# Kernel tuning notes

Measured on AMD Instinct MI355X. Metric: run time of the kernel, lower is better.

Reference implementation:

```python
import jax, jax.numpy as jnp
import numpy as np

NHEAD = 4
LAYER_TYPES = ["self", "cross", "self", "cross", "semantic_subspace_cross"]


def _ln(x):
    m = jnp.mean(x, axis=-1, keepdims=True)
    v = jnp.var(x, axis=-1, keepdims=True)
    return (x - m) / jnp.sqrt(v + 1e-5)


def _attn(x, source, q_mask, kv_mask, qW, kW, vW, mW, w1, w2):
    # Faithful GeometryAttentionLayer forward (pe=None, sinusoidal branch).
    bs, L, C = x.shape
    dim = C // NHEAD
    qw = (x @ qW).reshape(bs, L, NHEAD, dim)
    kw = (source @ kW).reshape(bs, -1, NHEAD, dim)
    vw = (source @ vW).reshape(bs, -1, NHEAD, dim)
    a = jnp.einsum('nlhd,nshd->nlsh', qw, kw)
    if q_mask is not None:
        bad = q_mask[:, :, None, None] & (~kv_mask)[:, None, :, None]
        a = jnp.where(bad, -jnp.inf, a)
    a = jax.nn.softmax(a / jnp.sqrt(jnp.asarray(dim, x.dtype)), axis=2)
    o = jnp.einsum('nlsh,nshd->nlhd', a, vw).reshape(bs, L, C)
    msg = _ln(o @ mW)
    h = jnp.concatenate([x, msg], axis=-1)
    msg = _ln(jnp.maximum(h @ w1, 0.0) @ w2)
    return x + msg


def setup_inputs() -> dict:
    key = jax.random.key(0)
    ks = jax.random.split(key, 24)
    B, N, C, D2 = 2, 2048, 256, 384
    G, Lp, nL = 16, 512, len(LAYER_TYPES)
    inp = {
        'src_feat': jax.random.normal(ks[0], (B, N, C), jnp.float32),
        'tgt_feat': jax.random.normal(ks[1], (B, N, C), jnp.float32),
        's_pcd': jax.random.normal(ks[2], (B, N, 3), jnp.float32),
        't_pcd': jax.random.normal(ks[3], (B, N, 3), jnp.float32),
        'src_mask': jnp.ones((B, N), bool),
        'tgt_mask': jnp.ones((B, N), bool),
        'src_sub_ind_padded': jax.random.randint(ks[4], (G, Lp), 0, N + 1),
        'tgt_sub_ind_padded': jax.random.randint(ks[5], (G, Lp), 0, N + 1),
        'src_sub_ind_padded_mask': jnp.ones((G, Lp), bool),
        'tgt_sub_ind_padded_mask': jnp.ones((G, Lp), bool),
        'semantic_masks_valid': jnp.ones((G,), bool),
        'src_2dfeat': jax.random.normal(ks[6], (B, N, D2), jnp.float32),
        'tgt_2dfeat': jax.random.normal(ks[7], (B, N, D2), jnp.float32),
        'data': 0,
        'dinoW': jax.random.normal(ks[8], (D2, C), jnp.float32) / np.sqrt(D2),
        'qW': jax.random.normal(ks[9], (nL, C, C), jnp.float32) / np.sqrt(C),
        'kW': jax.random.normal(ks[10], (nL, C, C), jnp.float32) / np.sqrt(C),
        'vW': jax.random.normal(ks[11], (nL, C, C), jnp.float32) / np.sqrt(C),
        'mW': jax.random.normal(ks[12], (nL, C, C), jnp.float32) / np.sqrt(C),
        'w1': jax.random.normal(ks[13], (nL, 2 * C, 2 * C), jnp.float32) / np.sqrt(2 * C),
        'w2': jax.random.normal(ks[14], (nL, 2 * C, C), jnp.float32) / np.sqrt(2 * C),
    }
    return inp


def reference(src_feat, tgt_feat, s_pcd, t_pcd, src_mask, tgt_mask,
              src_sub_ind_padded, tgt_sub_ind_padded,
              src_sub_ind_padded_mask, tgt_sub_ind_padded_mask,
              semantic_masks_valid, src_2dfeat, tgt_2dfeat, data,
              dinoW, qW, kW, vW, mW, w1, w2):
    src2 = src_2dfeat @ dinoW
    tgt2 = tgt_2dfeat @ dinoW
    s_sem = t_sem = None
    for i, name in enumerate(LAYER_TYPES):
        P = (qW[i], kW[i], vW[i], mW[i], w1[i], w2[i])
        if name == 'self':
            src_feat = src_feat + src2
            tgt_feat = tgt_feat + tgt2
            src_feat = _attn(src_feat, src_feat, src_mask, src_mask, *P)
            tgt_feat = _attn(tgt_feat, tgt_feat, tgt_mask, tgt_mask, *P)
        elif name == 'cross':
            src_feat = _attn(src_feat, tgt_feat, src_mask, tgt_mask, *P)
            tgt_feat = _attn(tgt_feat, src_feat, tgt_mask, src_mask, *P)
        else:  # semantic_subspace_cross
            B, N, C = src_feat.shape
            G = src_sub_ind_padded.shape[0]
            mask_num = G // B
            se = jnp.repeat(src_feat[:, None], mask_num, axis=1).reshape(G, N, C)
            te = jnp.repeat(tgt_feat[:, None], mask_num, axis=1).reshape(G, N, C)
            # boolean-select valid semantic groups (all valid in this config,
            # so fixed-size nonzero is exact)
            vidx = jnp.nonzero(semantic_masks_valid, size=G, fill_value=0)[0]
            se, te = se[vidx], te[vidx]
            si, ti = src_sub_ind_padded[vidx], tgt_sub_ind_padded[vidx]
            sm, tm = src_sub_ind_padded_mask[vidx], tgt_sub_ind_padded_mask[vidx]
            # append zero row so pad index N gathers zeros
            se = jnp.concatenate([se, jnp.zeros_like(se[:, :1])], axis=1)
            te = jnp.concatenate([te, jnp.zeros_like(te[:, :1])], axis=1)
            ssub = jnp.take_along_axis(se, si[:, :, None], axis=1)
            tsub = jnp.take_along_axis(te, ti[:, :, None], axis=1)
            s_sem = _attn(ssub, tsub, ~sm, ~tm, *P)
            t_sem = _attn(tsub, ssub, ~tm, ~sm, *P)
    return (src_feat, tgt_feat, s_sem, t_sem)
```

## Files before the change

kernel.cpp:

```cpp
#include <hip/hip_runtime.h>
#include <hip/hip_bf16.h>
#include <cstdint>
#include <cstddef>


typedef __attribute__((ext_vector_type(8))) short bf16x8;
typedef __attribute__((ext_vector_type(4))) float f32x4;

__device__ __forceinline__ float b2f(unsigned short u) {
  union { unsigned int i; float f; } v; v.i = ((unsigned int)u) << 16; return v.f;
}
__device__ __forceinline__ unsigned short f2b(float f) {
  __hip_bfloat16 h = __float2bfloat16(f);
  union { __hip_bfloat16 h; unsigned short u; } v; v.h = h; return v.u;
}
__device__ __forceinline__ unsigned int pk2(float a, float b) {
  return (unsigned int)f2b(a) | ((unsigned int)f2b(b) << 16);
}
__device__ __forceinline__ float fexp2(float x) {
#if __has_builtin(__builtin_amdgcn_exp2f)
  return __builtin_amdgcn_exp2f(x);
#else
  float r; asm("v_exp_f32 %0, %1" : "=v"(r) : "v"(x)); return r;
#endif
}

__global__ __launch_bounds__(256) void k_probe(int* __restrict__ flag,
                                               const unsigned short* __restrict__ w,
                                               int n) {
  __shared__ int ok[256];
  const int t = threadIdx.x;
  int good = 1;
  for (int i = t; i < n; i += 256) {
    float v = fabsf(b2f(w[i]));
    if (!(v < 1e3f)) good = 0;
  }
  ok[t] = good;
  __syncthreads();
  for (int s = 128; s; s >>= 1) {
    if (t < s) ok[t] &= ok[t + s];
    __syncthreads();
  }
  if (t == 0) *flag = ok[0];
}

__global__ __launch_bounds__(256) void k_load2(float* __restrict__ dF,
                                               unsigned short* __restrict__ dB,
                                               const void* __restrict__ src,
                                               int n4, const int* __restrict__ flag) {
  int i = blockIdx.x * 256 + threadIdx.x;
  if (i >= n4) return;
  float4 f;
  if (*flag) {
    ushort4 u = ((const ushort4*)src)[i];
    f.x = b2f(u.x); f.y = b2f(u.y); f.z = b2f(u.z); f.w = b2f(u.w);
  } else {
    f = ((const float4*)src)[i];
  }
  ((float4*)dF)[i] = f;
  ushort4 o; o.x = f2b(f.x); o.y = f2b(f.y); o.z = f2b(f.z); o.w = f2b(f.w);
  ((ushort4*)dB)[i] = o;
}

__global__ __launch_bounds__(256) void k_loadb(unsigned short* __restrict__ dB,
                                               const void* __restrict__ src,
                                               int n4, const int* __restrict__ flag) {
  int i = blockIdx.x * 256 + threadIdx.x;
  if (i >= n4) return;
  if (*flag) {
    ((ushort4*)dB)[i] = ((const ushort4*)src)[i];
    return;
  }
  float4 f = ((const float4*)src)[i];
  ushort4 o; o.x = f2b(f.x); o.y = f2b(f.y); o.z = f2b(f.z); o.w = f2b(f.w);
  ((ushort4*)dB)[i] = o;
}

__global__ __launch_bounds__(256) void k_store(void* __restrict__ out, size_t off,
                                               const float* __restrict__ src,
                                               int n4, const int* __restrict__ flag) {
  int i = blockIdx.x * 256 + threadIdx.x;
  if (i >= n4) return;
  float4 f = ((const float4*)src)[i];
  if (*flag) {
    ushort4 u; u.x = f2b(f.x); u.y = f2b(f.y); u.z = f2b(f.z); u.w = f2b(f.w);
    ((ushort4*)((unsigned short*)out + off))[i] = u;
  } else {
    ((float4*)((float*)out + off))[i] = f;
  }
}

__global__ __launch_bounds__(256) void k_add_dino(float* __restrict__ xF,
                                                  unsigned short* __restrict__ xB,
                                                  const unsigned short* __restrict__ addB,
                                                  int n4) {
  int i = blockIdx.x * 256 + threadIdx.x;
  if (i >= n4) return;
  float4 a = ((const float4*)xF)[i];
  ushort4 u = ((const ushort4*)addB)[i];
  a.x += b2f(u.x); a.y += b2f(u.y); a.z += b2f(u.z); a.w += b2f(u.w);
  ((float4*)xF)[i] = a;
  ushort4 o; o.x = f2b(a.x); o.y = f2b(a.y); o.z = f2b(a.z); o.w = f2b(a.w);
  ((ushort4*)xB)[i] = o;
}

__global__ __launch_bounds__(256) void k_wt(unsigned short* __restrict__ Wt,
                                            const void* __restrict__ W,
                                            int K, int N, int zStride,
                                            const int* __restrict__ flag) {
  __shared__ float tile[32][33];
  const int isbf = *flag;
  const int z = blockIdx.z;
  const unsigned short* Wb = (const unsigned short*)W + (size_t)z * K * N;
  const float* Wf = (const float*)W + (size_t)z * K * N;
  unsigned short* Wo = Wt + (size_t)z * zStride;
  const int KS = K >> 5;
  const int nx = blockIdx.x * 32, ky = blockIdx.y * 32;
  const int tx = threadIdx.x & 31, ty = threadIdx.x >> 5;
#pragma unroll
  for (int i = 0; i < 4; ++i) {
    int k = ky + ty + i * 8;
    float v = isbf ? b2f(Wb[(size_t)k * N + nx + tx]) : Wf[(size_t)k * N + nx + tx];
    tile[ty + i * 8][tx] = v;
  }
  __syncthreads();
  const int kstep = ky >> 5;
  const int lanehi = (tx >> 3) << 4;
  const int e = tx & 7;
#pragma unroll
  for (int i = 0; i < 4; ++i) {
    int nn = ty + i * 8;
    int n_ = nx + nn;
    size_t idx = ((((size_t)(n_ >> 4) * KS + kstep) << 6) + (lanehi + (n_ & 15))) * 8 + e;
    Wo[idx] = f2b(tile[tx][nn]);
  }
}

template<int KTOT>
__global__ __launch_bounds__(256, 4) void k_gmm(unsigned short* __restrict__ Y, int ldy,
                                                const unsigned short* __restrict__ A1, int lda1,
                                                const unsigned short* __restrict__ A2, int lda2,
                                                int K1,
                                                const unsigned short* __restrict__ Wt,
                                                int relu, int rowOff, int rowXor,
                                                int xorColStart, int qkvLog2L) {
  constexpr int KS = KTOT >> 5;
  const int tid = threadIdx.x;
  const int wq = tid >> 6, lane = tid & 63;
  const int l16 = lane & 15, quad = lane >> 4;
  const int gx = gridDim.x;
  const int nwg = gx * gridDim.y;
  const int lid = blockIdx.y * gx + blockIdx.x;
  const int w = (lid & 7) * (nwg >> 3) + (lid >> 3);
  const int n0 = (w % gx) * 64, m0 = (w / gx) * 64;
  const int row = m0 + wq * 16 + l16;
  int arow = rowOff + row;
  if (n0 >= xorColStart) arow ^= rowXor;

  const unsigned short* Wb0 = Wt + ((size_t)(n0 >> 4) * KS << 6) * 8 + (size_t)lane * 8;

  f32x4 acc[4];
#pragma unroll
  for (int i = 0; i < 4; ++i) acc[i] = (f32x4){0.f, 0.f, 0.f, 0.f};

  auto ldA = [&](int k0) -> bf16x8 {
    const unsigned short* ap = (k0 < K1)
        ? (A1 + (size_t)arow * lda1 + k0)
        : (A2 + (size_t)arow * lda2 + (k0 - K1));
    return *(const bf16x8*)(ap + quad * 8);
  };
  auto ldB = [&](int k0, int nb) -> bf16x8 {
    return *(const bf16x8*)(Wb0 + ((size_t)nb * KS + (k0 >> 5)) * 512);
  };

  bf16x8 a0 = ldA(0), a1;
  bf16x8 b0[4], b1[4];
#pragma unroll
  for (int nb = 0; nb < 4; ++nb) b0[nb] = ldB(0, nb);

#pragma unroll
  for (int k0 = 0; k0 < KTOT; k0 += 64) {
    a1 = ldA(k0 + 32);
#pragma unroll
    for (int nb = 0; nb < 4; ++nb) b1[nb] = ldB(k0 + 32, nb);
#pragma unroll
    for (int nb = 0; nb < 4; ++nb)
      acc[nb] = __builtin_amdgcn_mfma_f32_16x16x32_bf16(a0, b0[nb], acc[nb], 0, 0, 0);
    if (k0 + 64 < KTOT) {
      a0 = ldA(k0 + 64);
#pragma unroll
      for (int nb = 0; nb < 4; ++nb) b0[nb] = ldB(k0 + 64, nb);
    }
#pragma unroll
    for (int nb = 0; nb < 4; ++nb)
      acc[nb] = __builtin_amdgcn_mfma_f32_16x16x32_bf16(a1, b1[nb], acc[nb], 0, 0, 0);
  }

  if (qkvLog2L) {
    const int Lm = (1 << qkvLog2L) - 1;
    const int sel = n0 >> 8;
    const int hh = (n0 >> 6) & 3;
    unsigned short* base = Y + (size_t)sel * ((size_t)gridDim.y << 14);
#pragma unroll
    for (int r = 0; r < 4; ++r) {
      const int rr = m0 + wq * 16 + quad * 4 + r;
      const int tok = rr & Lm;
      const int hi = ((rr >> qkvLog2L) << 2) + hh;
      unsigned short* yp = base + ((((size_t)hi << qkvLog2L) + tok) << 6) + l16;
#pragma unroll
      for (int nb = 0; nb < 4; ++nb) yp[nb * 16] = f2b(acc[nb][r]);
    }
  } else {
#pragma unroll
    for (int r = 0; r < 4; ++r) {
      unsigned short* yp = Y + (size_t)(m0 + wq * 16 + quad * 4 + r) * ldy + n0;
#pragma unroll
      for (int nb = 0; nb < 4; ++nb) {
        float v = acc[nb][r];
        if (relu) v = fmaxf(v, 0.f);
        yp[nb * 16 + l16] = f2b(v);
      }
    }
  }
}

__device__ __forceinline__ void row_stats(float4 v, float& mean, float& inv) {
  float s  = v.x + v.y + v.z + v.w;
  float s2 = fmaf(v.x, v.x, fmaf(v.y, v.y, fmaf(v.z, v.z, v.w * v.w)));
#pragma unroll
  for (int off = 32; off >= 1; off >>= 1) {
    s  += __shfl_xor(s,  off, 64);
    s2 += __shfl_xor(s2, off, 64);
  }
  mean = s * (1.f / 256.f);
  float var = s2 * (1.f / 256.f) - mean * mean;
  inv = rsqrtf(var + 1e-5f);
}

template<int KTOT>
__global__ __launch_bounds__(256, 4) void k_gmm_ln(unsigned short* __restrict__ Yb,
                                                   float* __restrict__ xF,
                                                   void* __restrict__ outp, size_t outOff,
                                                   const unsigned short* __restrict__ xBres,
                                                   const unsigned short* __restrict__ A1,
                                                   int lda1,
                                                   const unsigned short* __restrict__ Wt,
                                                   int mode, const int* __restrict__ flag) {
  constexpr int KS = KTOT >> 5;
  __shared__ float Ot[16][260];
  const int tid = threadIdx.x;
  const int wq = tid >> 6, lane = tid & 63;
  const int l16 = lane & 15, quad = lane >> 4;
  const int nwg = gridDim.x;
  const int lid = blockIdx.x;
  const int w = (lid & 7) * (nwg >> 3) + (lid >> 3);
  const int R0 = w * 16;

  const unsigned short* Wb0 = Wt + ((size_t)(wq * 4) * KS << 6) * 8 + (size_t)lane * 8;
  const unsigned short* Ap = A1 + (size_t)(R0 + l16) * lda1;

  f32x4 acc[4];
#pragma unroll
  for (int i = 0; i < 4; ++i) acc[i] = (f32x4){0.f, 0.f, 0.f, 0.f};

  auto ldA = [&](int k0) -> bf16x8 { return *(const bf16x8*)(Ap + k0 + quad * 8); };
  auto ldB = [&](int k0, int nb) -> bf16x8 {
    return *(const bf16x8*)(Wb0 + ((size_t)nb * KS + (k0 >> 5)) * 512);
  };

  bf16x8 a0 = ldA(0), a1;
  bf16x8 b0[4], b1[4];
#pragma unroll
  for (int nb = 0; nb < 4; ++nb) b0[nb] = ldB(0, nb);

#pragma unroll
  for (int k0 = 0; k0 < KTOT; k0 += 64) {
    a1 = ldA(k0 + 32);
#pragma unroll
    for (int nb = 0; nb < 4; ++nb) b1[nb] = ldB(k0 + 32, nb);
#pragma unroll
    for (int nb = 0; nb < 4; ++nb)
      acc[nb] = __builtin_amdgcn_mfma_f32_16x16x32_bf16(a0, b0[nb], acc[nb], 0, 0, 0);
    if (k0 + 64 < KTOT) {
      a0 = ldA(k0 + 64);
#pragma unroll
      for (int nb = 0; nb < 4; ++nb) b0[nb] = ldB(k0 + 64, nb);
    }
#pragma unroll
    for (int nb = 0; nb < 4; ++nb)
      acc[nb] = __builtin_amdgcn_mfma_f32_16x16x32_bf16(a1, b1[nb], acc[nb], 0, 0, 0);
  }

#pragma unroll
  for (int nb = 0; nb < 4; ++nb)
#pragma unroll
    for (int r = 0; r < 4; ++r)
      Ot[quad * 4 + r][wq * 64 + nb * 16 + l16] = acc[nb][r];
  __syncthreads();

#pragma unroll
  for (int rr = 0; rr < 4; ++rr) {
    const int row = rr * 4 + wq;
    float4 v = *(const float4*)&Ot[row][lane * 4];
    float mean, inv; row_stats(v, mean, inv);
    float4 nv;
    nv.x = (v.x - mean) * inv; nv.y = (v.y - mean) * inv;
    nv.z = (v.z - mean) * inv; nv.w = (v.w - mean) * inv;
    const size_t gr = (size_t)(R0 + row) * 256 + lane * 4;
    if (mode == 1) {
      float4 xv = *(const float4*)(xF + gr);
      float4 rs;
      rs.x = xv.x + nv.x; rs.y = xv.y + nv.y; rs.z = xv.z + nv.z; rs.w = xv.w + nv.w;
      *(float4*)(xF + gr) = rs;
      ushort4 u; u.x = f2b(rs.x); u.y = f2b(rs.y); u.z = f2b(rs.z); u.w = f2b(rs.w);
      *(ushort4*)(Yb + gr) = u;
    } else {
      ushort4 xu = *(const ushort4*)(xBres + gr);
      float4 rs;
      rs.x = b2f(xu.x) + nv.x; rs.y = b2f(xu.y) + nv.y;
      rs.z = b2f(xu.z) + nv.z; rs.w = b2f(xu.w) + nv.w;
      if (*flag) {
        ushort4 u; u.x = f2b(rs.x); u.y = f2b(rs.y); u.z = f2b(rs.z); u.w = f2b(rs.w);
        *(ushort4*)((unsigned short*)outp + outOff + gr) = u;
      } else {
        *(float4*)((float*)outp + outOff + gr) = rs;
      }
    }
  }
}

__global__ __launch_bounds__(256, 4) void k_mprojc(unsigned short* __restrict__ msgB,
                                                   const float* __restrict__ pO,
                                                   const float* __restrict__ pML,
                                                   int lgL, int split, int NHt,
                                                   const unsigned short* __restrict__ Wt) {
  constexpr int KS = 8;
  __shared__ __align__(16) char smem[16640];
  unsigned short* At = (unsigned short*)smem;
  float (*Ot)[260] = (float (*)[260])smem;
  const int tid = threadIdx.x;
  const int wq = tid >> 6, lane = tid & 63;
  const int l16 = lane & 15, quad = lane >> 4;
  const int nwg = gridDim.x;
  const int lid = blockIdx.x;
  const int w = (lid & 7) * (nwg >> 3) + (lid >> 3);
  const int R0 = w * 16;
  const int L = 1 << lgL, Lm = L - 1;

  {
    const int i = tid >> 4;
    const int c = tid & 15;
    const int gr = R0 + i;
    const int n = gr >> lgL;
    const int tok = gr & Lm;
    const int nh = n * 4 + (c >> 2);
    float M = -1e30f;
    for (int sp = 0; sp < split; ++sp)
      M = fmaxf(M, pML[(((size_t)sp * NHt + nh) * L + tok) * 2]);
    float4 a0 = {0,0,0,0}, a1 = {0,0,0,0}, a2 = {0,0,0,0}, a3 = {0,0,0,0};
    float lsum = 0.f;
    for (int sp = 0; sp < split; ++sp) {
      const float* pml = pML + (((size_t)sp * NHt + nh) * L + tok) * 2;
      float e = fexp2(pml[0] - M);
      lsum = fmaf(pml[1], e, lsum);
      const float4* po = (const float4*)(pO + (((size_t)sp * NHt + nh) * L + tok) * 64
                                         + (c & 3) * 16);
      float4 v0 = po[0], v1 = po[1], v2 = po[2], v3 = po[3];
      a0.x = fmaf(v0.x, e, a0.x); a0.y = fmaf(v0.y, e, a0.y);
      a0.z = fmaf(v0.z, e, a0.z); a0.w = fmaf(v0.w, e, a0.w);
      a1.x = fmaf(v1.x, e, a1.x); a1.y = fmaf(v1.y, e, a1.y);
      a1.z = fmaf(v1.z, e, a1.z); a1.w = fmaf(v1.w, e, a1.w);
      a2.x = fmaf(v2.x, e, a2.x); a2.y = fmaf(v2.y, e, a2.y);
      a2.z = fmaf(v2.z, e, a2.z); a2.w = fmaf(v2.w, e, a2.w);
      a3.x = fmaf(v3.x, e, a3.x); a3.y = fmaf(v3.y, e, a3.y);
      a3.z = fmaf(v3.z, e, a3.z); a3.w = fmaf(v3.w, e, a3.w);
    }
    float inv = 1.0f / lsum;
    union { unsigned short us[8]; uint4 v; } p0, p1;
    p0.us[0] = f2b(a0.x * inv); p0.us[1] = f2b(a0.y * inv);
    p0.us[2] = f2b(a0.z * inv); p0.us[3] = f2b(a0.w * inv);
    p0.us[4] = f2b(a1.x * inv); p0.us[5] = f2b(a1.y * inv);
    p0.us[6] = f2b(a1.z * inv); p0.us[7] = f2b(a1.w * inv);
    p1.us[0] = f2b(a2.x * inv); p1.us[1] = f2b(a2.y * inv);
    p1.us[2] = f2b(a2.z * inv); p1.us[3] = f2b(a2.w * inv);
    p1.us[4] = f2b(a3.x * inv); p1.us[5] = f2b(a3.y * inv);
    p1.us[6] = f2b(a3.z * inv); p1.us[7] = f2b(a3.w * inv);
    const int u0 = (2 * c) ^ (i & 7);
    const int u1 = (2 * c + 1) ^ (i & 7);
    *(uint4*)&At[((i << 5) + u0) * 8] = p0.v;
    *(uint4*)&At[((i << 5) + u1) * 8] = p1.v;
  }
  __syncthreads();

  const unsigned short* Wb0 = Wt + ((size_t)(wq * 4) * KS << 6) * 8 + (size_t)lane * 8;
  f32x4 acc[4];
#pragma unroll
  for (int i = 0; i < 4; ++i) acc[i] = (f32x4){0.f, 0.f, 0.f, 0.f};

  auto ldA = [&](int k0) -> bf16x8 {
    const int u = (k0 >> 3) + quad;
    return *(const bf16x8*)&At[((l16 << 5) + (u ^ (l16 & 7))) * 8];
  };
  auto ldB = [&](int k0, int nb) -> bf16x8 {
    return *(const bf16x8*)(Wb0 + ((size_t)nb * KS + (k0 >> 5)) * 512);
  };

  bf16x8 b0[4], b1[4];
#pragma unroll
  for (int nb = 0; nb < 4; ++nb) b0[nb] = ldB(0, nb);
#pragma unroll
  for (int k0 = 0; k0 < 256; k0 += 64) {
#pragma unroll
    for (int nb = 0; nb < 4; ++nb) b1[nb] = ldB(k0 + 32, nb);
    bf16x8 a0 = ldA(k0);
#pragma unroll
    for (int nb = 0; nb < 4; ++nb)
      acc[nb] = __builtin_amdgcn_mfma_f32_16x16x32_bf16(a0, b0[nb], acc[nb], 0, 0, 0);
    if (k0 + 64 < 256) {
#pragma unroll
      for (int nb = 0; nb < 4; ++nb) b0[nb] = ldB(k0 + 64, nb);
    }
    bf16x8 a1 = ldA(k0 + 32);
#pragma unroll
    for (int nb = 0; nb < 4; ++nb)
      acc[nb] = __builtin_amdgcn_mfma_f32_16x16x32_bf16(a1, b1[nb], acc[nb], 0, 0, 0);
  }
  __syncthreads();

#pragma unroll
  for (int nb = 0; nb < 4; ++nb)
#pragma unroll
    for (int r = 0; r < 4; ++r)
      Ot[quad * 4 + r][wq * 64 + nb * 16 + l16] = acc[nb][r];
  __syncthreads();

#pragma unroll
  for (int rr = 0; rr < 4; ++rr) {
    const int row = rr * 4 + wq;
    float4 v = *(const float4*)&Ot[row][lane * 4];
    float mean, inv; row_stats(v, mean, inv);
    ushort4 u;
    u.x = f2b((v.x - mean) * inv); u.y = f2b((v.y - mean) * inv);
    u.z = f2b((v.z - mean) * inv); u.w = f2b((v.w - mean) * inv);
    *(ushort4*)(msgB + (size_t)(R0 + row) * 256 + lane * 4) = u;
  }
}

__global__ __launch_bounds__(512, 4) void k_attn_p(float* __restrict__ pO,
                                                   float* __restrict__ pML,
                                                   const unsigned short* __restrict__ QKV,
                                                   unsigned long long kOff,
                                                   int L, int S, int chunk) {
  __shared__ __align__(16) char smem[34816];
  unsigned short* Kl = (unsigned short*)smem;
  unsigned short (*Vt)[64][72] = (unsigned short (*)[64][72])(smem + 16384);
  const int tid = threadIdx.x;
  const int wq = tid >> 6, lane = tid & 63;
  const int l16 = lane & 15, quad = lane >> 4;
  const int q0 = blockIdx.x * 256;
  const int nh = blockIdx.y, NHt = gridDim.y;
  const int s0 = blockIdx.z * chunk;
  const float S2 = 0.18033688f;

  const unsigned short* Qh = QKV + (size_t)nh * L * 64;
  const unsigned short* Kh = QKV + kOff + (size_t)nh * S * 64;
  const unsigned short* Vh = QKV + 2 * kOff + (size_t)nh * S * 64;

  bf16x8 qa[2][2];
#pragma unroll
  for (int qb = 0; qb < 2; ++qb) {
    const unsigned short* qp = Qh + (size_t)(q0 + (qb * 8 + wq) * 16 + l16) * 64;
    qa[qb][0] = *(const bf16x8*)(qp + quad * 8);
    qa[qb][1] = *(const bf16x8*)(qp + 32 + quad * 8);
  }

  const short ONE = (short)0x3F80;
  const bf16x8 onesv = (bf16x8){ONE, ONE, ONE, ONE, ONE, ONE, ONE, ONE};

  f32x4 acc[2][4];
  f32x4 lacc[2];
#pragma unroll
  for (int qb = 0; qb < 2; ++qb) {
#pragma unroll
    for (int i = 0; i < 4; ++i) acc[qb][i] = (f32x4){0.f, 0.f, 0.f, 0.f};
    lacc[qb] = (f32x4){0.f, 0.f, 0.f, 0.f};
  }
  float m_[2] = {-1e30f, -1e30f};

  const int skey = tid >> 3;
  const int sdh0 = (tid & 7) * 8;
  const int kidx = (((skey >> 4) * 2 + (sdh0 >> 5)) * 64 +
                    (((sdh0 >> 3) & 3) * 16) + ((skey & 15) ^ (tid & 7))) * 8;
  const int krd0 = lane ^ quad;
  const int krd1 = lane ^ (4 | quad);
  const int vdh0 = wq * 8;
  const int pc = ((lane >> 5) << 5) + (((lane >> 2) & 3) << 3)
               + (((lane >> 4) & 1) << 2) + (lane & 3);

  uint4 kv = *(const uint4*)(Kh + (size_t)(s0 + skey) * 64 + sdh0);
  uint4 va = *(const uint4*)(Vh + (size_t)(s0 + lane) * 64 + vdh0);
  *(uint4*)&Kl[kidx] = kv;
  {
    const unsigned short* pv = (const unsigned short*)&va;
#pragma unroll
    for (int i = 0; i < 8; ++i) Vt[0][vdh0 + i][pc] = pv[i];
  }
  if (chunk > 64) {
    kv = *(const uint4*)(Kh + (size_t)(s0 + 64 + skey) * 64 + sdh0);
    va = *(const uint4*)(Vh + (size_t)(s0 + 64 + lane) * 64 + vdh0);
  }
  __syncthreads();

  int cur = 0;
  for (int t = 0; t < chunk; t += 64) {
    f32x4 sc[2][4];
    const unsigned short* Klc = Kl + cur * 4096;
    __builtin_amdgcn_s_setprio(1);
#pragma unroll
    for (int kb = 0; kb < 4; ++kb) {
      bf16x8 kf0 = *(const bf16x8*)&Klc[((kb * 2 + 0) * 64 + krd0) * 8];
      bf16x8 kf1 = *(const bf16x8*)&Klc[((kb * 2 + 1) * 64 + krd1) * 8];
#pragma unroll
      for (int qb = 0; qb < 2; ++qb) {
        f32x4 z = (f32x4){0.f, 0.f, 0.f, 0.f};
        z = __builtin_amdgcn_mfma_f32_16x16x32_bf16(kf0, qa[qb][0], z, 0, 0, 0);
        z = __builtin_amdgcn_mfma_f32_16x16x32_bf16(kf1, qa[qb][1], z, 0, 0, 0);
        sc[qb][kb] = z;
      }
    }
    __builtin_amdgcn_s_setprio(0);
    if (t + 64 < chunk) {
      *(uint4*)&Kl[(cur ^ 1) * 4096 + kidx] = kv;
      const unsigned short* pv = (const unsigned short*)&va;
#pragma unroll
      for (int i = 0; i < 8; ++i) Vt[cur ^ 1][vdh0 + i][pc] = pv[i];
    }
    if (t + 128 < chunk) {
      kv = *(const uint4*)(Kh + (size_t)(s0 + t + 128 + skey) * 64 + sdh0);
      va = *(const uint4*)(Vh + (size_t)(s0 + t + 128 + lane) * 64 + vdh0);
    }
    union { bf16x8 v; unsigned int w[4]; } ps0[2], ps1[2];
#pragma unroll
    for (int qb = 0; qb < 2; ++qb) {
      f32x4 mv01, mv;
#pragma unroll
      for (int r = 0; r < 4; ++r) mv01[r] = fmaxf(sc[qb][0][r], sc[qb][1][r]);
#pragma unroll
      for (int r = 0; r < 4; ++r) mv[r] = fmaxf(mv01[r], fmaxf(sc[qb][2][r], sc[qb][3][r]));
      float mx = fmaxf(fmaxf(mv[0], mv[1]), fmaxf(mv[2], mv[3])) * S2;
      mx = fmaxf(mx, __shfl_xor(mx, 16));
      mx = fmaxf(mx, __shfl_xor(mx, 32));
      float mn;
      if (__all(mx <= m_[qb] + 8.f)) {
        mn = m_[qb];
      } else {
        mn = fmaxf(m_[qb], mx);
        float alpha = fexp2(m_[qb] - mn);
        m_[qb] = mn;
#pragma unroll
        for (int r = 0; r < 4; ++r) lacc[qb][r] *= alpha;
#pragma unroll
        for (int nb = 0; nb < 4; ++nb)
#pragma unroll
          for (int r = 0; r < 4; ++r) acc[qb][nb][r] *= alpha;
      }
#pragma unroll
      for (int kb = 0; kb < 4; ++kb)
#pragma unroll
        for (int r = 0; r < 4; ++r)
          sc[qb][kb][r] = fexp2(fmaf(sc[qb][kb][r], S2, -mn));
      ps0[qb].w[0] = pk2(sc[qb][0][0], sc[qb][0][1]);
      ps0[qb].w[1] = pk2(sc[qb][0][2], sc[qb][0][3]);
      ps0[qb].w[2] = pk2(sc[qb][1][0], sc[qb][1][1]);
      ps0[qb].w[3] = pk2(sc[qb][1][2], sc[qb][1][3]);
      ps1[qb].w[0] = pk2(sc[qb][2][0], sc[qb][2][1]);
      ps1[qb].w[1] = pk2(sc[qb][2][2], sc[qb][2][3]);
      ps1[qb].w[2] = pk2(sc[qb][3][0], sc[qb][3][1]);
      ps1[qb].w[3] = pk2(sc[qb][3][2], sc[qb][3][3]);
    }
    __builtin_amdgcn_s_setprio(1);
#pragma unroll
    for (int db = 0; db < 4; ++db) {
      bf16x8 vb0 = *(const bf16x8*)&Vt[cur][db * 16 + l16][quad * 8];
      bf16x8 vb1 = *(const bf16x8*)&Vt[cur][db * 16 + l16][32 + quad * 8];
#pragma unroll
      for (int qb = 0; qb < 2; ++qb) {
        acc[qb][db] = __builtin_amdgcn_mfma_f32_16x16x32_bf16(vb0, ps0[qb].v, acc[qb][db], 0, 0, 0);
        acc[qb][db] = __builtin_amdgcn_mfma_f32_16x16x32_bf16(vb1, ps1[qb].v, acc[qb][db], 0, 0, 0);
      }
    }
#pragma unroll
    for (int qb = 0; qb < 2; ++qb) {
      lacc[qb] = __builtin_amdgcn_mfma_f32_16x16x32_bf16(onesv, ps0[qb].v, lacc[qb], 0, 0, 0);
      lacc[qb] = __builtin_amdgcn_mfma_f32_16x16x32_bf16(onesv, ps1[qb].v, lacc[qb], 0, 0, 0);
    }
    __builtin_amdgcn_s_setprio(0);
    __syncthreads();
    cur ^= 1;
  }

  float* Ot = (float*)smem;
#pragma unroll
  for (int qb = 0; qb < 2; ++qb) {
#pragma unroll
    for (int pass = 0; pass < 2; ++pass) {
      __syncthreads();
      if ((wq >> 2) == pass) {
#pragma unroll
        for (int db = 0; db < 4; ++db)
          *(f32x4*)&Ot[(size_t)((wq & 3) * 16 + l16) * 68 + db * 16 + quad * 4] = acc[qb][db];
      }
      __syncthreads();
      if ((wq >> 2) == pass) {
#pragma unroll
        for (int i = 0; i < 16; ++i) {
          const int row = q0 + (qb * 8 + wq) * 16 + i;
          pO[((size_t)(blockIdx.z * NHt + nh) * L + row) * 64 + lane] =
              Ot[(size_t)((wq & 3) * 16 + i) * 68 + lane];
        }
      }
    }
  }
  if (quad == 0) {
#pragma unroll
    for (int qb = 0; qb < 2; ++qb) {
      float* pml = pML + ((size_t)(blockIdx.z * NHt + nh) * L +
                          q0 + (qb * 8 + wq) * 16 + l16) * 2;
      pml[0] = m_[qb]; pml[1] = lacc[qb][0];
    }
  }
}

__global__ __launch_bounds__(256) void k_gather2(unsigned short* __restrict__ dst,
                                                 const float* __restrict__ sF,
                                                 const int* __restrict__ sIdx,
                                                 const int* __restrict__ tIdx) {
  const int row = blockIdx.x * 4 + (threadIdx.x >> 6);
  const int t = threadIdx.x & 63;
  const int half = row >> 13;
  const int r = row & 8191;
  const int g = r >> 9;
  const int b = g >> 3;
  const int id = half ? tIdx[r] : sIdx[r];
  float4 v = {0.f, 0.f, 0.f, 0.f};
  if ((unsigned)id < 2048u) {
    const float* base = sF + (size_t)(half * 2 + b) * 524288;
    v = ((const float4*)(base + (size_t)id * 256))[t];
  }
  ushort4 u; u.x = f2b(v.x); u.y = f2b(v.y); u.z = f2b(v.z); u.w = f2b(v.w);
  ((ushort4*)(dst + (size_t)row * 256))[t] = u;
}

extern "C" void kernel_launch(void* const* d_in, const int* in_sizes, int n_in,
                              void* d_out, int out_size, void* d_ws, size_t ws_size,
                              hipStream_t stream) {
  const void* src_feat = d_in[0];
  const void* tgt_feat = d_in[1];
  const int* s_sub = (const int*)d_in[6];
  const int* t_sub = (const int*)d_in[7];
  const void* src2d = d_in[11];
  const void* tgt2d = d_in[12];
  const void* dinoW = d_in[14];
  const void* qW = d_in[15];
  const void* kW = d_in[16];
  const void* vW = d_in[17];
  const void* mW = d_in[18];
  const void* w1 = d_in[19];
  const void* w2 = d_in[20];

  const int BIG = 1 << 30;
  char* p = (char*)d_ws;
  int* dflag = (int*)p;                       p += 256;
  float* sF = (float*)p;                      p += 4194304;
  float* tF = (float*)p;                      p += 4194304;
  unsigned short* sB    = (unsigned short*)p; p += 2097152;
  unsigned short* tB    = (unsigned short*)p; p += 2097152;
  unsigned short* s2B   = (unsigned short*)p; p += 2097152;
  unsigned short* t2B   = (unsigned short*)p; p += 2097152;
  unsigned short* d2B   = (unsigned short*)p; p += 3145728;
  unsigned short* sSubB = (unsigned short*)p; p += 4194304;
  unsigned short* tSubB = (unsigned short*)p; p += 4194304;
  unsigned short* qkvB  = (unsigned short*)p;
  unsigned short* msgB  = (unsigned short*)(p + 8388608);
  p += 25165824;
  unsigned short* hB    = (unsigned short*)p;
  p += 25165824;
  unsigned short* WtD   = (unsigned short*)p; p += 196608;
  unsigned short* WtQKV = (unsigned short*)p; p += 1966080;
  unsigned short* WtM   = (unsigned short*)p; p += 655360;
  unsigned short* WtW1  = (unsigned short*)p; p += 2621440;
  unsigned short* WtW2  = (unsigned short*)p; p += 1310720;
  float* pO  = (float*)p;                     p += 33554432;
  float* pML = (float*)p;                     p += 2097152;

  k_probe<<<1, 256, 0, stream>>>(dflag, (const unsigned short*)qW, 4096);

  k_wt<<<dim3(8, 12, 1), 256, 0, stream>>>(WtD, dinoW, 384, 256, 0, dflag);
  k_wt<<<dim3(8, 8, 5), 256, 0, stream>>>(WtQKV,          qW, 256, 256, 196608, dflag);
  k_wt<<<dim3(8, 8, 5), 256, 0, stream>>>(WtQKV + 65536,  kW, 256, 256, 196608, dflag);
  k_wt<<<dim3(8, 8, 5), 256, 0, stream>>>(WtQKV + 131072, vW, 256, 256, 196608, dflag);
  k_wt<<<dim3(8, 8, 5), 256, 0, stream>>>(WtM, mW, 256, 256, 65536, dflag);
  k_wt<<<dim3(16, 16, 5), 256, 0, stream>>>(WtW1, w1, 512, 512, 262144, dflag);
  k_wt<<<dim3(8, 16, 5), 256, 0, stream>>>(WtW2, w2, 512, 256, 131072, dflag);

  auto attnB = [&](int l, const unsigned short* Abase, int rowOff, int rowXor,
                   int M, int L, int S, int split, int NHt,
                   float* xF, unsigned short* xB, size_t outOff) {
    const int lg = (L == 2048) ? 11 : 9;
    k_gmm<256><<<dim3(12, M / 64), 256, 0, stream>>>(
        qkvB, 768, Abase, 256, Abase, 256, 256,
        WtQKV + (size_t)l * 196608, 0, rowOff, rowXor, 256, lg);
    const int chunk = S / split;
    k_attn_p<<<dim3(L / 256, NHt, split), 512, 0, stream>>>(
        pO, pML, qkvB, (unsigned long long)M * 256, L, S, chunk);
    k_mprojc<<<M / 16, 256, 0, stream>>>(msgB, pO, pML, lg, split, NHt,
                                         WtM + (size_t)l * 65536);
    k_gmm<512><<<dim3(8, M / 64), 256, 0, stream>>>(
        hB, 512, xB, 256, msgB, 256, 256, WtW1 + (size_t)l * 262144, 1, 0, 0, BIG, 0);
    if (xF) k_gmm_ln<512><<<M / 16, 256, 0, stream>>>(
        xB, xF, nullptr, 0, nullptr, hB, 512, WtW2 + (size_t)l * 131072, 1, dflag);
    else    k_gmm_ln<512><<<M / 16, 256, 0, stream>>>(
        nullptr, nullptr, d_out, outOff, xB, hB, 512, WtW2 + (size_t)l * 131072, 2, dflag);
  };

  k_load2<<<1024, 256, 0, stream>>>(sF, sB, src_feat, 262144, dflag);
  k_load2<<<1024, 256, 0, stream>>>(tF, tB, tgt_feat, 262144, dflag);
  k_loadb<<<1536, 256, 0, stream>>>(d2B, src2d, 393216, dflag);
  k_gmm<384><<<dim3(4, 64), 256, 0, stream>>>(s2B, 256, d2B, 384, d2B, 384, 384,
                                              WtD, 0, 0, 0, BIG, 0);
  k_loadb<<<1536, 256, 0, stream>>>(d2B, tgt2d, 393216, dflag);
  k_gmm<384><<<dim3(4, 64), 256, 0, stream>>>(t2B, 256, d2B, 384, d2B, 384, 384,
                                              WtD, 0, 0, 0, BIG, 0);

  k_add_dino<<<2048, 256, 0, stream>>>(sF, sB, s2B, 524288);
  attnB(0, sB, 0, 0, 8192, 2048, 2048, 4, 16, sF, sB, 0);
  attnB(1, sB, 0,    4096, 4096, 2048, 2048, 8, 8, sF, sB, 0);
  attnB(1, sB, 4096, 4096, 4096, 2048, 2048, 8, 8, tF, tB, 0);
  k_add_dino<<<2048, 256, 0, stream>>>(sF, sB, s2B, 524288);
  attnB(2, sB, 0, 0, 8192, 2048, 2048, 4, 16, sF, sB, 0);
  attnB(3, sB, 0,    4096, 4096, 2048, 2048, 8, 8, sF, sB, 0);
  attnB(3, sB, 4096, 4096, 4096, 2048, 2048, 8, 8, tF, tB, 0);
  k_gather2<<<4096, 256, 0, stream>>>(sSubB, sF, s_sub, t_sub);
  attnB(4, sSubB, 0, 8192, 16384, 512, 512, 2, 128, nullptr, sSubB, 2097152);

  k_store<<<2048, 256, 0, stream>>>(d_out, 0, sF, 524288, dflag);
}
```

Baseline: 738.1 us.

## Give each wave a full 16x256 row tile so layernorm runs in registers

The two GEMM+layernorm kernels now have each wave compute 16 rows across all 256 output columns, so a block covers 64 rows instead of 16. Row statistics are reduced in registers with 16-lane shuffles, which removes the LDS staging buffer and its barrier before the layernorm. The aim is to reuse each A fragment across 16 N-blocks and drop the shared-memory round trip. In exchange there are 64 accumulator registers per lane, the old double-buffered prefetch is gone, the grid is four times smaller, and the output stores become scalar 2- and 4-byte writes instead of vector stores.

```diff
diff --git a/kernel.cpp b/kernel.cpp
--- a/kernel.cpp
+++ b/kernel.cpp
@@ -224,11 +224,19 @@
   }
 }
 
-__device__ __forceinline__ void row_stats(float4 v, float& mean, float& inv) {
-  float s  = v.x + v.y + v.z + v.w;
-  float s2 = fmaf(v.x, v.x, fmaf(v.y, v.y, fmaf(v.z, v.z, v.w * v.w)));
-#pragma unroll
-  for (int off = 32; off >= 1; off >>= 1) {
+__device__ __forceinline__ void ln_reg(const f32x4 acc[4][4], int r,
+                                       float& mean, float& inv) {
+  float s = 0.f, s2 = 0.f;
+#pragma unroll
+  for (int cb = 0; cb < 4; ++cb)
+#pragma unroll
+    for (int nb = 0; nb < 4; ++nb) {
+      float v = acc[cb][nb][r];
+      s += v;
+      s2 = fmaf(v, v, s2);
+    }
+#pragma unroll
+  for (int off = 8; off >= 1; off >>= 1) {
     s  += __shfl_xor(s,  off, 64);
     s2 += __shfl_xor(s2, off, 64);
   }
@@ -247,85 +255,58 @@
                                                    const unsigned short* __restrict__ Wt,
                                                    int mode, const int* __restrict__ flag) {
   constexpr int KS = KTOT >> 5;
-  __shared__ float Ot[16][260];
   const int tid = threadIdx.x;
   const int wq = tid >> 6, lane = tid & 63;
   const int l16 = lane & 15, quad = lane >> 4;
   const int nwg = gridDim.x;
   const int lid = blockIdx.x;
   const int w = (lid & 7) * (nwg >> 3) + (lid >> 3);
-  const int R0 = w * 16;
-
-  const unsigned short* Wb0 = Wt + ((size_t)(wq * 4) * KS << 6) * 8 + (size_t)lane * 8;
-  const unsigned short* Ap = A1 + (size_t)(R0 + l16) * lda1;
-
-  f32x4 acc[4];
-#pragma unroll
-  for (int i = 0; i < 4; ++i) acc[i] = (f32x4){0.f, 0.f, 0.f, 0.f};
-
-  auto ldA = [&](int k0) -> bf16x8 { return *(const bf16x8*)(Ap + k0 + quad * 8); };
-  auto ldB = [&](int k0, int nb) -> bf16x8 {
-    return *(const bf16x8*)(Wb0 + ((size_t)nb * KS + (k0 >> 5)) * 512);
-  };
-
-  bf16x8 a0 = ldA(0), a1;
-  bf16x8 b0[4], b1[4];
-#pragma unroll
-  for (int nb = 0; nb < 4; ++nb) b0[nb] = ldB(0, nb);
-
-#pragma unroll
-  for (int k0 = 0; k0 < KTOT; k0 += 64) {
-    a1 = ldA(k0 + 32);
-#pragma unroll
-    for (int nb = 0; nb < 4; ++nb) b1[nb] = ldB(k0 + 32, nb);
-#pragma unroll
-    for (int nb = 0; nb < 4; ++nb)
-      acc[nb] = __builtin_amdgcn_mfma_f32_16x16x32_bf16(a0, b0[nb], acc[nb], 0, 0, 0);
-    if (k0 + 64 < KTOT) {
-      a0 = ldA(k0 + 64);
-#pragma unroll
-      for (int nb = 0; nb < 4; ++nb) b0[nb] = ldB(k0 + 64, nb);
-    }
-#pragma unroll
-    for (int nb = 0; nb < 4; ++nb)
-      acc[nb] = __builtin_amdgcn_mfma_f32_16x16x32_bf16(a1, b1[nb], acc[nb], 0, 0, 0);
-  }
-
-#pragma unroll
-  for (int nb = 0; nb < 4; ++nb)
-#pragma unroll
-    for (int r = 0; r < 4; ++r)
-      Ot[quad * 4 + r][wq * 64 + nb * 16 + l16] = acc[nb][r];
-  __syncthreads();
-
-#pragma unroll
-  for (int rr = 0; rr < 4; ++rr) {
-    const int row = rr * 4 + wq;
-    float4 v = *(const float4*)&Ot[row][lane * 4];
-    float mean, inv; row_stats(v, mean, inv);
-    float4 nv;
-    nv.x = (v.x - mean) * inv; nv.y = (v.y - mean) * inv;
-    nv.z = (v.z - mean) * inv; nv.w = (v.w - mean) * inv;
-    const size_t gr = (size_t)(R0 + row) * 256 + lane * 4;
-    if (mode == 1) {
-      float4 xv = *(const float4*)(xF + gr);
-      float4 rs;
-      rs.x = xv.x + nv.x; rs.y = xv.y + nv.y; rs.z = xv.z + nv.z; rs.w = xv.w + nv.w;
-      *(float4*)(xF + gr) = rs;
-      ushort4 u; u.x = f2b(rs.x); u.y = f2b(rs.y); u.z = f2b(rs.z); u.w = f2b(rs.w);
-      *(ushort4*)(Yb + gr) = u;
-    } else {
-      ushort4 xu = *(const ushort4*)(xBres + gr);
-      float4 rs;
-      rs.x = b2f(xu.x) + nv.x; rs.y = b2f(xu.y) + nv.y;
-      rs.z = b2f(xu.z) + nv.z; rs.w = b2f(xu.w) + nv.w;
-      if (*flag) {
-        ushort4 u; u.x = f2b(rs.x); u.y = f2b(rs.y); u.z = f2b(rs.z); u.w = f2b(rs.w);
-        *(ushort4*)((unsigned short*)outp + outOff + gr) = u;
-      } else {
-        *(float4*)((float*)outp + outOff + gr) = rs;
-      }
-    }
+  const int R0 = w * 64;
+
+  const unsigned short* Ap = A1 + (size_t)(R0 + wq * 16 + l16) * lda1;
+  const unsigned short* Wb0 = Wt + (size_t)lane * 8;
+
+  f32x4 acc[4][4];
+#pragma unroll
+  for (int cb = 0; cb < 4; ++cb)
+#pragma unroll
+    for (int nb = 0; nb < 4; ++nb) acc[cb][nb] = (f32x4){0.f, 0.f, 0.f, 0.f};
+
+#pragma unroll
+  for (int cb = 0; cb < 4; ++cb) {
+#pragma unroll
+    for (int k0 = 0; k0 < KTOT; k0 += 32) {
+      bf16x8 a = *(const bf16x8*)(Ap + k0 + quad * 8);
+#pragma unroll
+      for (int nb = 0; nb < 4; ++nb) {
+        bf16x8 b = *(const bf16x8*)(Wb0 +
+            (((size_t)(cb * 4 + nb) * KS + (k0 >> 5)) << 9));
+        acc[cb][nb] = __builtin_amdgcn_mfma_f32_16x16x32_bf16(a, b, acc[cb][nb], 0, 0, 0);
+      }
+    }
+  }
+
+#pragma unroll
+  for (int r = 0; r < 4; ++r) {
+    float mean, inv;
+    ln_reg(acc, r, mean, inv);
+    const int row = R0 + wq * 16 + quad * 4 + r;
+#pragma unroll
+    for (int cb = 0; cb < 4; ++cb)
+#pragma unroll
+      for (int nb = 0; nb < 4; ++nb) {
+        const float nv = (acc[cb][nb][r] - mean) * inv;
+        const size_t gr = (size_t)row * 256 + cb * 64 + nb * 16 + l16;
+        if (mode == 1) {
+          float rs = xF[gr] + nv;
+          xF[gr] = rs;
+          Yb[gr] = f2b(rs);
+        } else {
+          float rs = b2f(xBres[gr]) + nv;
+          if (*flag) ((unsigned short*)outp)[outOff + gr] = f2b(rs);
+          else       ((float*)outp)[outOff + gr] = rs;
+        }
+      }
   }
 }
 
@@ -335,20 +316,19 @@
                                                    int lgL, int split, int NHt,
                                                    const unsigned short* __restrict__ Wt) {
   constexpr int KS = 8;
-  __shared__ __align__(16) char smem[16640];
-  unsigned short* At = (unsigned short*)smem;
-  float (*Ot)[260] = (float (*)[260])smem;
+  __shared__ __align__(16) unsigned short At[64 * 32 * 8];
   const int tid = threadIdx.x;
   const int wq = tid >> 6, lane = tid & 63;
   const int l16 = lane & 15, quad = lane >> 4;
   const int nwg = gridDim.x;
   const int lid = blockIdx.x;
   const int w = (lid & 7) * (nwg >> 3) + (lid >> 3);
-  const int R0 = w * 16;
+  const int R0 = w * 64;
   const int L = 1 << lgL, Lm = L - 1;
 
-  {
-    const int i = tid >> 4;
+#pragma unroll
+  for (int it = 0; it < 4; ++it) {
+    const int i = it * 16 + (tid >> 4);
     const int c = tid & 15;
     const int gr = R0 + i;
     const int n = gr >> lgL;
@@ -392,57 +372,40 @@
   }
   __syncthreads();
 
-  const unsigned short* Wb0 = Wt + ((size_t)(wq * 4) * KS << 6) * 8 + (size_t)lane * 8;
-  f32x4 acc[4];
-#pragma unroll
-  for (int i = 0; i < 4; ++i) acc[i] = (f32x4){0.f, 0.f, 0.f, 0.f};
-
-  auto ldA = [&](int k0) -> bf16x8 {
-    const int u = (k0 >> 3) + quad;
-    return *(const bf16x8*)&At[((l16 << 5) + (u ^ (l16 & 7))) * 8];
-  };
-  auto ldB = [&](int k0, int nb) -> bf16x8 {
-    return *(const bf16x8*)(Wb0 + ((size_t)nb * KS + (k0 >> 5)) * 512);
-  };
-
-  bf16x8 b0[4], b1[4];
-#pragma unroll
-  for (int nb = 0; nb < 4; ++nb) b0[nb] = ldB(0, nb);
-#pragma unroll
-  for (int k0 = 0; k0 < 256; k0 += 64) {
-#pragma unroll
-    for (int nb = 0; nb < 4; ++nb) b1[nb] = ldB(k0 + 32, nb);
-    bf16x8 a0 = ldA(k0);
-#pragma unroll
-    for (int nb = 0; nb < 4; ++nb)
-      acc[nb] = __builtin_amdgcn_mfma_f32_16x16x32_bf16(a0, b0[nb], acc[nb], 0, 0, 0);
-    if (k0 + 64 < 256) {
-#pragma unroll
-      for (int nb = 0; nb < 4; ++nb) b0[nb] = ldB(k0 + 64, nb);
-    }
-    bf16x8 a1 = ldA(k0 + 32);
-#pragma unroll
-    for (int nb = 0; nb < 4; ++nb)
-      acc[nb] = __builtin_amdgcn_mfma_f32_16x16x32_bf16(a1, b1[nb], acc[nb], 0, 0, 0);
-  }
-  __syncthreads();
-
-#pragma unroll
-  for (int nb = 0; nb < 4; ++nb)
-#pragma unroll
-    for (int r = 0; r < 4; ++r)
-      Ot[quad * 4 + r][wq * 64 + nb * 16 + l16] = acc[nb][r];
-  __syncthreads();
-
-#pragma unroll
-  for (int rr = 0; rr < 4; ++rr) {
-    const int row = rr * 4 + wq;
-    float4 v = *(const float4*)&Ot[row][lane * 4];
-    float mean, inv; row_stats(v, mean, inv);
-    ushort4 u;
-    u.x = f2b((v.x - mean) * inv); u.y = f2b((v.y - mean) * inv);
-    u.z = f2b((v.z - mean) * inv); u.w = f2b((v.w - mean) * inv);
-    *(ushort4*)(msgB + (size_t)(R0 + row) * 256 + lane * 4) = u;
+  const unsigned short* Wb0 = Wt + (size_t)lane * 8;
+  const int arow = wq * 16 + l16;
+  f32x4 acc[4][4];
+#pragma unroll
+  for (int cb = 0; cb < 4; ++cb)
+#pragma unroll
+    for (int nb = 0; nb < 4; ++nb) acc[cb][nb] = (f32x4){0.f, 0.f, 0.f, 0.f};
+
+#pragma unroll
+  for (int cb = 0; cb < 4; ++cb) {
+#pragma unroll
+    for (int k0 = 0; k0 < 256; k0 += 32) {
+      const int u = (k0 >> 3) + quad;
+      bf16x8 a = *(const bf16x8*)&At[((arow << 5) + (u ^ (l16 & 7))) * 8];
+#pragma unroll
+      for (int nb = 0; nb < 4; ++nb) {
+        bf16x8 b = *(const bf16x8*)(Wb0 +
+            (((size_t)(cb * 4 + nb) * KS + (k0 >> 5)) << 9));
+        acc[cb][nb] = __builtin_amdgcn_mfma_f32_16x16x32_bf16(a, b, acc[cb][nb], 0, 0, 0);
+      }
+    }
+  }
+
+#pragma unroll
+  for (int r = 0; r < 4; ++r) {
+    float mean, inv;
+    ln_reg(acc, r, mean, inv);
+    const int row = R0 + wq * 16 + quad * 4 + r;
+#pragma unroll
+    for (int cb = 0; cb < 4; ++cb)
+#pragma unroll
+      for (int nb = 0; nb < 4; ++nb)
+        msgB[(size_t)row * 256 + cb * 64 + nb * 16 + l16] =
+            f2b((acc[cb][nb][r] - mean) * inv);
   }
 }
 
@@ -713,13 +676,13 @@
     const int chunk = S / split;
     k_attn_p<<<dim3(L / 256, NHt, split), 512, 0, stream>>>(
         pO, pML, qkvB, (unsigned long long)M * 256, L, S, chunk);
-    k_mprojc<<<M / 16, 256, 0, stream>>>(msgB, pO, pML, lg, split, NHt,
+    k_mprojc<<<M / 64, 256, 0, stream>>>(msgB, pO, pML, lg, split, NHt,
                                          WtM + (size_t)l * 65536);
     k_gmm<512><<<dim3(8, M / 64), 256, 0, stream>>>(
         hB, 512, xB, 256, msgB, 256, 256, WtW1 + (size_t)l * 262144, 1, 0, 0, BIG, 0);
-    if (xF) k_gmm_ln<512><<<M / 16, 256, 0, stream>>>(
+    if (xF) k_gmm_ln<512><<<M / 64, 256, 0, stream>>>(
         xB, xF, nullptr, 0, nullptr, hB, 512, WtW2 + (size_t)l * 131072, 1, dflag);
-    else    k_gmm_ln<512><<<M / 16, 256, 0, stream>>>(
+    else    k_gmm_ln<512><<<M / 64, 256, 0, stream>>>(
         nullptr, nullptr, d_out, outOff, xB, hB, 512, WtW2 + (size_t)l * 131072, 2, dflag);
   };
 
```

After: 1.260 ms. 70.7% more time.
